# Kernel tuning notes

Hardware: AMD Instinct MI355X
Metric: run time of the kernel (lower is better)

Reference implementation:

```python
import jax, jax.numpy as jnp
import numpy as np

N, E, G, T = 4096, 16384, 128, 100
DIMS = [(5, 64), (64, 128), (128, 256)]
EPS = 1e-5


def setup_inputs() -> dict:
    key = jax.random.key(0)
    ks = iter(jax.random.split(key, 64))
    d = {}
    d["x"] = jax.random.normal(next(ks), (N, 5), jnp.float32)
    d["edge_index"] = jax.random.randint(next(ks), (2, E), 0, N, jnp.int64)
    d["edge_attr"] = jax.random.uniform(next(ks), (E, 3), jnp.float32)
    d["batch_seg"] = jnp.sort(jax.random.randint(next(ks), (N,), 0, G, jnp.int64))
    for l, (cin, cout) in enumerate(DIMS, start=1):
        d[f"l{l}_W1"] = jax.random.normal(next(ks), (3, 32), jnp.float32) * 0.3
        d[f"l{l}_b1"] = jnp.zeros((32,), jnp.float32)
        d[f"l{l}_W2"] = jax.random.normal(next(ks), (32, cin * cout), jnp.float32) * 0.05
        d[f"l{l}_b2"] = jnp.zeros((cin * cout,), jnp.float32)
        d[f"l{l}_root"] = jax.random.normal(next(ks), (cin, cout), jnp.float32) * 0.1
        d[f"l{l}_bias"] = jnp.zeros((cout,), jnp.float32)
        d[f"bn{l}_g"] = jnp.ones((cout,), jnp.float32)
        d[f"bn{l}_b"] = jnp.zeros((cout,), jnp.float32)
        d[f"bn{l}_m"] = jax.random.normal(next(ks), (cout,), jnp.float32) * 0.01
        d[f"bn{l}_v"] = jax.random.uniform(next(ks), (cout,), jnp.float32, 0.5, 1.5)
    d["mlp_W"] = jax.random.normal(next(ks), (256, T), jnp.float32) * 0.06
    d["mlp_b"] = jnp.zeros((T,), jnp.float32)
    return d


def _nnconv(h, src, dst, edge_attr, W1, b1, W2, b2, root, bias, cin, cout):
    # edge MLP -> per-edge weight matrix [E, cin, cout]
    ew = (jax.nn.relu(edge_attr @ W1 + b1) @ W2 + b2).reshape(-1, cin, cout)
    msg = jnp.einsum('ei,eio->eo', h[src], ew)  # gather + per-edge matmul
    ssum = jax.ops.segment_sum(msg, dst, num_segments=N)
    cnt = jax.ops.segment_sum(jnp.ones((msg.shape[0],), msg.dtype), dst, num_segments=N)
    agg = ssum / jnp.maximum(cnt, 1.0)[:, None]  # scatter-mean
    return h @ root + agg + bias


def _bn(h, g, b, m, v):
    return g * (h - m) * jax.lax.rsqrt(v + EPS) + b


def reference(x, edge_index, edge_attr, batch_seg,
              l1_W1, l1_b1, l1_W2, l1_b2, l1_root, l1_bias, bn1_g, bn1_b, bn1_m, bn1_v,
              l2_W1, l2_b1, l2_W2, l2_b2, l2_root, l2_bias, bn2_g, bn2_b, bn2_m, bn2_v,
              l3_W1, l3_b1, l3_W2, l3_b2, l3_root, l3_bias, bn3_g, bn3_b, bn3_m, bn3_v,
              mlp_W, mlp_b):
    src, dst = edge_index[0], edge_index[1]
    h = _nnconv(x, src, dst, edge_attr, l1_W1, l1_b1, l1_W2, l1_b2, l1_root, l1_bias, 5, 64)
    h = jax.nn.relu(_bn(h, bn1_g, bn1_b, bn1_m, bn1_v))
    h = _nnconv(h, src, dst, edge_attr, l2_W1, l2_b1, l2_W2, l2_b2, l2_root, l2_bias, 64, 128)
    h = jax.nn.relu(_bn(h, bn2_g, bn2_b, bn2_m, bn2_v))
    h = _nnconv(h, src, dst, edge_attr, l3_W1, l3_b1, l3_W2, l3_b2, l3_root, l3_bias, 128, 256)
    h = jax.nn.relu(_bn(h, bn3_g, bn3_b, bn3_m, bn3_v))
    # global mean pool over graphs
    psum = jax.ops.segment_sum(h, batch_seg, num_segments=G)
    pcnt = jax.ops.segment_sum(jnp.ones((N,), h.dtype), batch_seg, num_segments=G)
    pooled = psum / jnp.maximum(pcnt, 1.0)[:, None]
    out = pooled @ mlp_W + mlp_b
    return jnp.where(out > 0, out, 0.1 * out)  # LeakyReLU(0.1)
```

## Files before the change

kernel.cpp:

```cpp
#include <hip/hip_runtime.h>
#include <cstdint>
#include <cstddef>

#define BN_EPS 1e-5f

typedef short bf16x8 __attribute__((ext_vector_type(8)));
typedef float f32x4  __attribute__((ext_vector_type(4)));
typedef unsigned short u16x8 __attribute__((ext_vector_type(8)));

__device__ __forceinline__ uint16_t f2bf_rte(float f) {
  uint32_t u = __float_as_uint(f);
  uint32_t r = u + 0x7fffu + ((u >> 16) & 1u);
  return (uint16_t)(r >> 16);
}
__device__ __forceinline__ float bf2f(uint16_t h) {
  return __uint_as_float(((uint32_t)h) << 16);
}
__device__ __forceinline__ void split_bf(float v, uint16_t& hi, uint16_t& lo) {
  hi = f2bf_rte(v);
  lo = f2bf_rte(v - bf2f(hi));
}

__global__ void zero_i32_k(int* p, int n) {
  int i = blockIdx.x * blockDim.x + threadIdx.x;
  if (i < n) p[i] = 0;
}

__global__ void hist_k(const int* __restrict__ dst, int* __restrict__ cnt, int E) {
  int e = blockIdx.x * blockDim.x + threadIdx.x;
  if (e < E) atomicAdd(&cnt[dst[e]], 1);
}

__global__ __launch_bounds__(1024) void scan_k(const int* __restrict__ cnt,
                                               int* __restrict__ offsets,
                                               int* __restrict__ cursor,
                                               int N, int total) {
  __shared__ int part[1024];
  int t = threadIdx.x;
  int a0 = cnt[4*t+0], a1 = cnt[4*t+1], a2 = cnt[4*t+2], a3 = cnt[4*t+3];
  part[t] = a0 + a1 + a2 + a3;
  __syncthreads();
  for (int off = 1; off < 1024; off <<= 1) {
    int v = (t >= off) ? part[t - off] : 0;
    __syncthreads();
    part[t] += v;
    __syncthreads();
  }
  int excl = (t == 0) ? 0 : part[t-1];
  int o0 = excl, o1 = o0 + a0, o2 = o1 + a1, o3 = o2 + a2;
  offsets[4*t+0] = o0; offsets[4*t+1] = o1; offsets[4*t+2] = o2; offsets[4*t+3] = o3;
  cursor [4*t+0] = o0; cursor [4*t+1] = o1; cursor [4*t+2] = o2; cursor [4*t+3] = o3;
  if (t == 0) offsets[N] = total;
}

__global__ void scatter_k(const int* __restrict__ dst, int* __restrict__ cursor,
                          int* __restrict__ csr, int E) {
  int e = blockIdx.x * blockDim.x + threadIdx.x;
  if (e < E) {
    int d = dst[e];
    int pos = atomicAdd(&cursor[d], 1);
    csr[pos] = e;
  }
}

__global__ void build_W2pT_k(const float* __restrict__ W2, const float* __restrict__ b2,
                             const float* __restrict__ root,
                             uint16_t* __restrict__ Bhi, uint16_t* __restrict__ Blo,
                             int cin, int cout, int Kpad) {
  int idx = blockIdx.x * blockDim.x + threadIdx.x;
  int total = cout * Kpad;
  if (idx >= total) return;
  int o  = idx / Kpad;
  int ki = idx - o * Kpad;
  float v = 0.f;
  if (ki < 34 * cin) {
    int k = ki / cin;
    int i = ki - k * cin;
    if (k < 32)       v = W2[(size_t)k * cin * cout + (size_t)i * cout + o];
    else if (k == 32) v = b2[(size_t)i * cout + o];
    else              v = root[(size_t)i * cout + o];
  }
  uint16_t hi, lo;
  split_bf(v, hi, lo);
  Bhi[idx] = hi;
  Blo[idx] = lo;
}

template<int CIN>
__global__ __launch_bounds__(256) void build_S_vec_k(const float* __restrict__ h,
                                                     const float* __restrict__ ea,
                                                     const float* __restrict__ W1,
                                                     const float* __restrict__ b1,
                                                     const int* __restrict__ src,
                                                     const int* __restrict__ csr,
                                                     const int* __restrict__ offsets,
                                                     uint16_t* __restrict__ Shi,
                                                     uint16_t* __restrict__ Slo,
                                                     int Kpad) {
  constexpr int CH = 8;
  constexpr int K1 = 33 * CIN;
  constexpr int NCH = K1 / 8;
  constexpr int NP = (NCH + 255) / 256;
  __shared__ float hs[CH][CIN];
  __shared__ float zs[CH][33];
  __shared__ int   es[CH];
  const int n = blockIdx.x;
  const int tid = threadIdx.x;
  const int base = offsets[n];
  const int deg  = offsets[n+1] - base;
  const float scale = 1.f / fmaxf((float)deg, 1.f);
  float acc[NP][8];
#pragma unroll
  for (int p = 0; p < NP; p++)
#pragma unroll
    for (int j = 0; j < 8; j++) acc[p][j] = 0.f;

  for (int c0 = 0; c0 < deg; c0 += CH) {
    const int cc = min(CH, deg - c0);
    if (tid < cc) es[tid] = csr[base + c0 + tid];
    __syncthreads();
    for (int idx = tid; idx < cc * CIN; idx += 256) {
      int slot = idx / CIN, i = idx - slot * CIN;
      hs[slot][i] = h[(size_t)src[es[slot]] * CIN + i];
    }
    for (int idx = tid; idx < cc * 33; idx += 256) {
      int slot = idx / 33, k = idx - slot * 33;
      float v;
      if (k == 32) v = 1.f;
      else {
        int e = es[slot];
        v = fmaxf(ea[e*3+0] * W1[k] + ea[e*3+1] * W1[32 + k] + ea[e*3+2] * W1[64 + k] + b1[k], 0.f);
      }
      zs[slot][k] = v;
    }
    __syncthreads();
#pragma unroll
    for (int p = 0; p < NP; p++) {
      int ch = p * 256 + tid;
      if (ch < NCH) {
        int ki0 = ch * 8;
        int k  = ki0 / CIN;
        int i0 = ki0 & (CIN - 1);
        for (int c = 0; c < cc; c++) {
          float zv = zs[c][k];
          float4 h0 = *(const float4*)&hs[c][i0];
          float4 h1 = *(const float4*)&hs[c][i0 + 4];
          acc[p][0] += zv * h0.x; acc[p][1] += zv * h0.y;
          acc[p][2] += zv * h0.z; acc[p][3] += zv * h0.w;
          acc[p][4] += zv * h1.x; acc[p][5] += zv * h1.y;
          acc[p][6] += zv * h1.z; acc[p][7] += zv * h1.w;
        }
      }
    }
    __syncthreads();
  }
  const size_t rowb = (size_t)n * Kpad;
#pragma unroll
  for (int p = 0; p < NP; p++) {
    int ch = p * 256 + tid;
    if (ch < NCH) {
      u16x8 hv, lv;
#pragma unroll
      for (int j = 0; j < 8; j++) {
        uint16_t hi, lo;
        split_bf(acc[p][j] * scale, hi, lo);
        hv[j] = hi; lv[j] = lo;
      }
      *(u16x8*)(Shi + rowb + ch * 8) = hv;
      *(u16x8*)(Slo + rowb + ch * 8) = lv;
    }
  }
  for (int c = tid; c < CIN / 8; c += 256) {
    int i0 = c * 8;
    float4 a = *(const float4*)&h[(size_t)n * CIN + i0];
    float4 b = *(const float4*)&h[(size_t)n * CIN + i0 + 4];
    float vals[8] = {a.x, a.y, a.z, a.w, b.x, b.y, b.z, b.w};
    u16x8 hv, lv;
#pragma unroll
    for (int j = 0; j < 8; j++) {
      uint16_t hi, lo;
      split_bf(vals[j], hi, lo);
      hv[j] = hi; lv[j] = lo;
    }
    *(u16x8*)(Shi + rowb + K1 + i0) = hv;
    *(u16x8*)(Slo + rowb + K1 + i0) = lv;
  }
  for (int ki = 34 * CIN + tid; ki < Kpad; ki += 256) {
    Shi[rowb + ki] = 0;
    Slo[rowb + ki] = 0;
  }
}

__global__ __launch_bounds__(256) void build_S5_k(const float* __restrict__ h,
                                                  const float* __restrict__ ea,
                                                  const float* __restrict__ W1,
                                                  const float* __restrict__ b1,
                                                  const int* __restrict__ src,
                                                  const int* __restrict__ csr,
                                                  const int* __restrict__ offsets,
                                                  uint16_t* __restrict__ Shi,
                                                  uint16_t* __restrict__ Slo,
                                                  int Kpad) {
  constexpr int CIN = 5, CH = 8;
  constexpr int K1 = 33 * CIN;
  constexpr int KT = 34 * CIN;
  __shared__ float hs[CH][CIN];
  __shared__ float zs[CH][33];
  __shared__ int   es[CH];
  const int n = blockIdx.x;
  const int tid = threadIdx.x;
  const int base = offsets[n];
  const int deg  = offsets[n+1] - base;
  const float scale = 1.f / fmaxf((float)deg, 1.f);
  float acc = 0.f;

  for (int c0 = 0; c0 < deg; c0 += CH) {
    const int cc = min(CH, deg - c0);
    if (tid < cc) es[tid] = csr[base + c0 + tid];
    __syncthreads();
    for (int idx = tid; idx < cc * CIN; idx += 256) {
      int slot = idx / CIN, i = idx - slot * CIN;
      hs[slot][i] = h[(size_t)src[es[slot]] * CIN + i];
    }
    for (int idx = tid; idx < cc * 33; idx += 256) {
      int slot = idx / 33, k = idx - slot * 33;
      float v;
      if (k == 32) v = 1.f;
      else {
        int e = es[slot];
        v = fmaxf(ea[e*3+0] * W1[k] + ea[e*3+1] * W1[32 + k] + ea[e*3+2] * W1[64 + k] + b1[k], 0.f);
      }
      zs[slot][k] = v;
    }
    __syncthreads();
    if (tid < K1) {
      int k = tid / CIN, i = tid - (tid / CIN) * CIN;
      float a = acc;
      for (int c = 0; c < cc; c++) a += zs[c][k] * hs[c][i];
      acc = a;
    }
    __syncthreads();
  }
  const size_t rowb = (size_t)n * Kpad;
  if (tid < K1) {
    uint16_t hi, lo;
    split_bf(acc * scale, hi, lo);
    Shi[rowb + tid] = hi;
    Slo[rowb + tid] = lo;
  }
  if (tid < CIN) {
    uint16_t hi, lo;
    split_bf(h[(size_t)n * CIN + tid], hi, lo);
    Shi[rowb + K1 + tid] = hi;
    Slo[rowb + K1 + tid] = lo;
  }
  for (int ki = KT + tid; ki < Kpad; ki += 256) {
    Shi[rowb + ki] = 0;
    Slo[rowb + ki] = 0;
  }
}

__global__ __launch_bounds__(256, 4) void mfma_gemm_sk_k(const uint16_t* __restrict__ Ahi,
                                                         const uint16_t* __restrict__ Alo,
                                                         const uint16_t* __restrict__ Bhi,
                                                         const uint16_t* __restrict__ Blo,
                                                         float* __restrict__ Cpart,
                                                         int Kpad, int Ncol, int M,
                                                         int itersPerSplit) {
  __shared__ uint16_t As[2][64][72];
  __shared__ uint16_t Bs[2][64][72];
  const int m0 = blockIdx.x * 64, n0 = blockIdx.y * 64;
  const int kbeg = blockIdx.z * itersPerSplit * 64;
  const int kend = min(Kpad, kbeg + itersPerSplit * 64);
  const int tid  = threadIdx.x;
  const int lane = tid & 63;
  const int wave = tid >> 6;
  const int wm = wave & 1, wn = wave >> 1;
  const int q  = lane >> 4;
  const int mr = lane & 15;

  f32x4 acc[2][2];
#pragma unroll
  for (int a = 0; a < 2; a++)
#pragma unroll
    for (int b = 0; b < 2; b++) acc[a][b] = (f32x4)0.f;

  for (int k0 = kbeg; k0 < kend; k0 += 64) {
#pragma unroll
    for (int rep = 0; rep < 2; rep++) {
      int chunk = rep * 256 + tid;
      int r = chunk >> 3, c = chunk & 7;
      size_t ga = (size_t)(m0 + r) * Kpad + k0 + c * 8;
      size_t gb = (size_t)(n0 + r) * Kpad + k0 + c * 8;
      *(uint4*)&As[0][r][c * 8] = *(const uint4*)(Ahi + ga);
      *(uint4*)&As[1][r][c * 8] = *(const uint4*)(Alo + ga);
      *(uint4*)&Bs[0][r][c * 8] = *(const uint4*)(Bhi + gb);
      *(uint4*)&Bs[1][r][c * 8] = *(const uint4*)(Blo + gb);
    }
    __syncthreads();
#pragma unroll
    for (int ks = 0; ks < 2; ks++) {
      const int kb = ks * 32 + q * 8;
      bf16x8 ah[2], al[2], bh[2], bl[2];
#pragma unroll
      for (int f = 0; f < 2; f++) {
        ah[f] = *(const bf16x8*)&As[0][wm * 32 + f * 16 + mr][kb];
        al[f] = *(const bf16x8*)&As[1][wm * 32 + f * 16 + mr][kb];
        bh[f] = *(const bf16x8*)&Bs[0][wn * 32 + f * 16 + mr][kb];
        bl[f] = *(const bf16x8*)&Bs[1][wn * 32 + f * 16 + mr][kb];
      }
#pragma unroll
      for (int fm = 0; fm < 2; fm++)
#pragma unroll
        for (int fn = 0; fn < 2; fn++) {
          acc[fm][fn] = __builtin_amdgcn_mfma_f32_16x16x32_bf16(ah[fm], bh[fn], acc[fm][fn], 0, 0, 0);
          acc[fm][fn] = __builtin_amdgcn_mfma_f32_16x16x32_bf16(ah[fm], bl[fn], acc[fm][fn], 0, 0, 0);
          acc[fm][fn] = __builtin_amdgcn_mfma_f32_16x16x32_bf16(al[fm], bh[fn], acc[fm][fn], 0, 0, 0);
        }
    }
    __syncthreads();
  }

  float* Cz = Cpart + (size_t)blockIdx.z * M * Ncol;
#pragma unroll
  for (int fm = 0; fm < 2; fm++) {
#pragma unroll
    for (int reg = 0; reg < 4; reg++) {
      int row = m0 + wm * 32 + fm * 16 + q * 4 + reg;
#pragma unroll
      for (int fn = 0; fn < 2; fn++) {
        int col = n0 + wn * 32 + fn * 16 + mr;
        Cz[(size_t)row * Ncol + col] = acc[fm][fn][reg];
      }
    }
  }
}

__global__ void epilogue_k(const float* __restrict__ Cpart, int SK, size_t plane4,
                           int Ncol,
                           const float* __restrict__ bias, const float* __restrict__ bg,
                           const float* __restrict__ bb, const float* __restrict__ bnm,
                           const float* __restrict__ bnv,
                           float* __restrict__ C, int total4) {
  int i = blockIdx.x * blockDim.x + threadIdx.x;
  if (i >= total4) return;
  float4 v = {0.f, 0.f, 0.f, 0.f};
  for (int z = 0; z < SK; z++) {
    float4 p = *((const float4*)Cpart + (size_t)z * plane4 + i);
    v.x += p.x; v.y += p.y; v.z += p.z; v.w += p.w;
  }
  int col0 = (i * 4) % Ncol;
  float o[4] = {v.x, v.y, v.z, v.w};
#pragma unroll
  for (int j = 0; j < 4; j++) {
    int c = col0 + j;
    float s = bg[c] * rsqrtf(bnv[c] + BN_EPS);
    float val = (o[j] + bias[c] - bnm[c]) * s + bb[c];
    o[j] = fmaxf(val, 0.f);
  }
  float4 r = {o[0], o[1], o[2], o[3]};
  *((float4*)C + i) = r;
}

__global__ __launch_bounds__(256) void pool_final_k(const float* __restrict__ h,
                                                    const int* __restrict__ seg,
                                                    const float* __restrict__ W,
                                                    const float* __restrict__ b,
                                                    float* __restrict__ out,
                                                    int N, int T) {
  __shared__ float pooled[256];
  const int g = blockIdx.x, tid = threadIdx.x;
  int lo = 0, hi = N;
  while (lo < hi) { int mid = (lo + hi) >> 1; if (seg[mid] < g) lo = mid + 1; else hi = mid; }
  int lo2 = lo, hi2 = N;
  while (lo2 < hi2) { int mid = (lo2 + hi2) >> 1; if (seg[mid] < g + 1) lo2 = mid + 1; else hi2 = mid; }
  const int cnt = lo2 - lo;
  const float inv = 1.f / fmaxf((float)cnt, 1.f);
  float s = 0.f;
  for (int n = lo; n < lo2; n++) s += h[(size_t)n * 256 + tid];
  pooled[tid] = s * inv;
  __syncthreads();
  if (tid < T) {
    float acc = b[tid];
    for (int o = 0; o < 256; o++) acc += pooled[o] * W[(size_t)o * T + tid];
    out[(size_t)g * T + tid] = (acc > 0.f) ? acc : 0.1f * acc;
  }
}

extern "C" void kernel_launch(void* const* d_in, const int* in_sizes, int n_in,
                              void* d_out, int out_size, void* d_ws, size_t ws_size,
                              hipStream_t stream) {
  const float* x   = (const float*)d_in[0];
  const int*   ei  = (const int*)d_in[1];
  const float* ea  = (const float*)d_in[2];
  const int*   seg = (const int*)d_in[3];

  const int N = in_sizes[0] / 5;
  const int E = in_sizes[2] / 3;
  const int T = in_sizes[35];
  const int G = out_size / T;
  const int* src = ei;
  const int* dst = ei + E;

  const float *W1[3], *b1[3], *W2[3], *b2[3], *root[3], *bias[3];
  const float *bng[3], *bnb[3], *bnm[3], *bnv[3];
  for (int l = 0; l < 3; l++) {
    int base = 4 + l * 10;
    W1[l]   = (const float*)d_in[base + 0];
    b1[l]   = (const float*)d_in[base + 1];
    W2[l]   = (const float*)d_in[base + 2];
    b2[l]   = (const float*)d_in[base + 3];
    root[l] = (const float*)d_in[base + 4];
    bias[l] = (const float*)d_in[base + 5];
    bng[l]  = (const float*)d_in[base + 6];
    bnb[l]  = (const float*)d_in[base + 7];
    bnm[l]  = (const float*)d_in[base + 8];
    bnv[l]  = (const float*)d_in[base + 9];
  }
  const float* mlpW = (const float*)d_in[34];
  const float* mlpb = (const float*)d_in[35];

  char* p = (char*)d_ws;
  auto carve = [&](size_t bytes) -> char* {
    char* r = p;
    p += (bytes + 255) & ~(size_t)255;
    return r;
  };
  const int KPADMAX = 4352;
  const int SKMAX = 8;
  int*      cnt     = (int*)carve((size_t)N * 4);
  int*      offsets = (int*)carve((size_t)(N + 1) * 4);
  int*      cursor  = (int*)carve((size_t)N * 4);
  int*      csr     = (int*)carve((size_t)E * 4);
  uint16_t* Whi     = (uint16_t*)carve((size_t)256 * KPADMAX * 2);
  uint16_t* Wlo     = (uint16_t*)carve((size_t)256 * KPADMAX * 2);
  uint16_t* Shi     = (uint16_t*)carve((size_t)N * KPADMAX * 2);
  uint16_t* Slo     = (uint16_t*)carve((size_t)N * KPADMAX * 2);
  float*    Cpart   = (float*)carve((size_t)SKMAX * N * 256 * 4 / 2);
  float*    hA      = (float*)carve((size_t)N * 256 * 4);
  float*    hB      = (float*)carve((size_t)N * 128 * 4);

  zero_i32_k<<<(N + 255) / 256, 256, 0, stream>>>(cnt, N);
  hist_k<<<(E + 255) / 256, 256, 0, stream>>>(dst, cnt, E);
  scan_k<<<1, 1024, 0, stream>>>(cnt, offsets, cursor, N, E);
  scatter_k<<<(E + 255) / 256, 256, 0, stream>>>(dst, cursor, csr, E);

  const int cins[3]  = {5, 64, 128};
  const int couts[3] = {64, 128, 256};
  const int kpads[3] = {192, 2176, 4352};
  const int sks[3]   = {1, 8, 4};
  const float* hin = x;
  float* houts[3] = {hB, hB, hA};
  houts[0] = hA; houts[1] = hB; houts[2] = hA;

  for (int l = 0; l < 3; l++) {
    int cin = cins[l], cout = couts[l], Kpad = kpads[l], SK = sks[l];
    int iters = Kpad / 64;
    int ips = (iters + SK - 1) / SK;
    build_W2pT_k<<<(cout * Kpad + 255) / 256, 256, 0, stream>>>(W2[l], b2[l], root[l],
                                                                Whi, Wlo, cin, cout, Kpad);
    if (cin == 5)
      build_S5_k<<<N, 256, 0, stream>>>(hin, ea, W1[l], b1[l], src, csr, offsets, Shi, Slo, Kpad);
    else if (cin == 64)
      build_S_vec_k<64><<<N, 256, 0, stream>>>(hin, ea, W1[l], b1[l], src, csr, offsets, Shi, Slo, Kpad);
    else
      build_S_vec_k<128><<<N, 256, 0, stream>>>(hin, ea, W1[l], b1[l], src, csr, offsets, Shi, Slo, Kpad);
    dim3 grid(N / 64, cout / 64, SK);
    mfma_gemm_sk_k<<<grid, 256, 0, stream>>>(Shi, Slo, Whi, Wlo, Cpart, Kpad, cout, N, ips);
    int total4 = N * cout / 4;
    epilogue_k<<<(total4 + 255) / 256, 256, 0, stream>>>(Cpart, SK, (size_t)N * cout / 4, cout,
                                                         bias[l], bng[l], bnb[l], bnm[l], bnv[l],
                                                         houts[l], total4);
    hin = houts[l];
  }

  pool_final_k<<<G, 256, 0, stream>>>(hA, seg, mlpW, mlpb, (float*)d_out, N, T);
}
```

Baseline: 285.8 us.

## Rewrite split-K MFMA GEMM with larger tiles, direct-to-LDS loads and double buffering

Replaces the 64x64 split-K bf16x3 GEMM with a templated 128xBN tile kernel. It stages A and B through global_load_lds into XOR-swizzled, double-buffered shared memory, so the next K-step's loads overlap the current MFMAs and each iteration needs one barrier instead of two. Split-K ranges are now divided evenly, and layer 1 uses split 3 so a smaller grid still fills the GPU. Larger tiles raise data reuse per load but increase register and LDS use, which lowers occupancy. The swizzle and the LDS-load addressing must match exactly for the results to be correct.

```diff
diff --git a/kernel.cpp b/kernel.cpp
--- a/kernel.cpp
+++ b/kernel.cpp
@@ -19,6 +19,12 @@
 __device__ __forceinline__ void split_bf(float v, uint16_t& hi, uint16_t& lo) {
   hi = f2bf_rte(v);
   lo = f2bf_rte(v - bf2f(hi));
+}
+
+__device__ __forceinline__ void glds16(const uint16_t* g, uint16_t* l) {
+  __builtin_amdgcn_global_load_lds(
+      (const __attribute__((address_space(1))) uint32_t*)(const void*)g,
+      (__attribute__((address_space(3))) uint32_t*)(void*)l, 16, 0, 0);
 }
 
 __global__ void zero_i32_k(int* p, int n) {
@@ -260,18 +266,33 @@
   }
 }
 
-__global__ __launch_bounds__(256, 4) void mfma_gemm_sk_k(const uint16_t* __restrict__ Ahi,
-                                                         const uint16_t* __restrict__ Alo,
-                                                         const uint16_t* __restrict__ Bhi,
-                                                         const uint16_t* __restrict__ Blo,
-                                                         float* __restrict__ Cpart,
-                                                         int Kpad, int Ncol, int M,
-                                                         int itersPerSplit) {
-  __shared__ uint16_t As[2][64][72];
-  __shared__ uint16_t Bs[2][64][72];
-  const int m0 = blockIdx.x * 64, n0 = blockIdx.y * 64;
-  const int kbeg = blockIdx.z * itersPerSplit * 64;
-  const int kend = min(Kpad, kbeg + itersPerSplit * 64);
+template<int BN>
+__global__ __launch_bounds__(256) void mfma_gemm2_k(const uint16_t* __restrict__ Ahi,
+                                                    const uint16_t* __restrict__ Alo,
+                                                    const uint16_t* __restrict__ Bhi,
+                                                    const uint16_t* __restrict__ Blo,
+                                                    float* __restrict__ Cpart,
+                                                    int Kpad, int Ncol, int M,
+                                                    int totalIters) {
+  constexpr int BM = 128;
+  constexpr int FN = BN / 32;
+  constexpr int NCA = BM / 32;
+  constexpr int NCB = BN / 32;
+  constexpr int OAH = 0;
+  constexpr int OAL = BM * 64;
+  constexpr int OBH = 2 * BM * 64;
+  constexpr int OBL = 2 * BM * 64 + BN * 64;
+  constexpr int BUFSZ = (2 * BM + 2 * BN) * 64;
+  __shared__ uint16_t smem[2 * BUFSZ] __attribute__((aligned(16)));
+
+  const int m0 = blockIdx.x * BM;
+  const int n0 = blockIdx.y * BN;
+  const int SK = gridDim.z;
+  const int z  = blockIdx.z;
+  const int itBeg = (int)((long long)totalIters * z / SK);
+  const int itEnd = (int)((long long)totalIters * (z + 1) / SK);
+  const int nsteps = itEnd - itBeg;
+
   const int tid  = threadIdx.x;
   const int lane = tid & 63;
   const int wave = tid >> 6;
@@ -279,61 +300,82 @@
   const int q  = lane >> 4;
   const int mr = lane & 15;
 
-  f32x4 acc[2][2];
-#pragma unroll
-  for (int a = 0; a < 2; a++)
-#pragma unroll
-    for (int b = 0; b < 2; b++) acc[a][b] = (f32x4)0.f;
-
-  for (int k0 = kbeg; k0 < kend; k0 += 64) {
-#pragma unroll
-    for (int rep = 0; rep < 2; rep++) {
-      int chunk = rep * 256 + tid;
-      int r = chunk >> 3, c = chunk & 7;
-      size_t ga = (size_t)(m0 + r) * Kpad + k0 + c * 8;
-      size_t gb = (size_t)(n0 + r) * Kpad + k0 + c * 8;
-      *(uint4*)&As[0][r][c * 8] = *(const uint4*)(Ahi + ga);
-      *(uint4*)&As[1][r][c * 8] = *(const uint4*)(Alo + ga);
-      *(uint4*)&Bs[0][r][c * 8] = *(const uint4*)(Bhi + gb);
-      *(uint4*)&Bs[1][r][c * 8] = *(const uint4*)(Blo + gb);
-    }
-    __syncthreads();
+  const int srow = tid >> 3;
+  const int swz  = ((tid & 7) ^ (srow & 7)) << 3;
+  size_t aoff[NCA], boff[NCB];
+#pragma unroll
+  for (int c = 0; c < NCA; c++)
+    aoff[c] = (size_t)(m0 + c * 32 + srow) * Kpad + swz + (size_t)itBeg * 64;
+#pragma unroll
+  for (int c = 0; c < NCB; c++)
+    boff[c] = (size_t)(n0 + c * 32 + srow) * Kpad + swz + (size_t)itBeg * 64;
+  const int wlds = wave << 9;
+
+  f32x4 acc[4][FN];
+#pragma unroll
+  for (int a = 0; a < 4; a++)
+#pragma unroll
+    for (int b = 0; b < FN; b++) acc[a][b] = (f32x4)0.f;
+
+  auto stage = [&](int buf, int t) {
+    uint16_t* base = smem + buf * BUFSZ;
+    const size_t ka = (size_t)t * 64;
+#pragma unroll
+    for (int c = 0; c < NCA; c++) {
+      glds16(Ahi + aoff[c] + ka, base + OAH + c * 2048 + wlds);
+      glds16(Alo + aoff[c] + ka, base + OAL + c * 2048 + wlds);
+    }
+#pragma unroll
+    for (int c = 0; c < NCB; c++) {
+      glds16(Bhi + boff[c] + ka, base + OBH + c * 2048 + wlds);
+      glds16(Blo + boff[c] + ka, base + OBL + c * 2048 + wlds);
+    }
+  };
+
+  if (nsteps > 0) stage(0, 0);
+  for (int t = 0; t < nsteps; t++) {
+    __syncthreads();
+    if (t + 1 < nsteps) stage((t & 1) ^ 1, t + 1);
+    const uint16_t* B_ = smem + (t & 1) * BUFSZ;
 #pragma unroll
     for (int ks = 0; ks < 2; ks++) {
-      const int kb = ks * 32 + q * 8;
-      bf16x8 ah[2], al[2], bh[2], bl[2];
-#pragma unroll
-      for (int f = 0; f < 2; f++) {
-        ah[f] = *(const bf16x8*)&As[0][wm * 32 + f * 16 + mr][kb];
-        al[f] = *(const bf16x8*)&As[1][wm * 32 + f * 16 + mr][kb];
-        bh[f] = *(const bf16x8*)&Bs[0][wn * 32 + f * 16 + mr][kb];
-        bl[f] = *(const bf16x8*)&Bs[1][wn * 32 + f * 16 + mr][kb];
-      }
-#pragma unroll
-      for (int fm = 0; fm < 2; fm++)
-#pragma unroll
-        for (int fn = 0; fn < 2; fn++) {
+      const int e0 = (ks * 32 + q * 8) ^ ((mr & 7) << 3);
+      bf16x8 ah[4], al[4], bh[FN], bl[FN];
+#pragma unroll
+      for (int f = 0; f < 4; f++) {
+        const int row = wm * 64 + f * 16 + mr;
+        ah[f] = *(const bf16x8*)&B_[OAH + row * 64 + e0];
+        al[f] = *(const bf16x8*)&B_[OAL + row * 64 + e0];
+      }
+#pragma unroll
+      for (int f = 0; f < FN; f++) {
+        const int row = wn * (BN / 2) + f * 16 + mr;
+        bh[f] = *(const bf16x8*)&B_[OBH + row * 64 + e0];
+        bl[f] = *(const bf16x8*)&B_[OBL + row * 64 + e0];
+      }
+#pragma unroll
+      for (int fm = 0; fm < 4; fm++)
+#pragma unroll
+        for (int fn = 0; fn < FN; fn++) {
           acc[fm][fn] = __builtin_amdgcn_mfma_f32_16x16x32_bf16(ah[fm], bh[fn], acc[fm][fn], 0, 0, 0);
           acc[fm][fn] = __builtin_amdgcn_mfma_f32_16x16x32_bf16(ah[fm], bl[fn], acc[fm][fn], 0, 0, 0);
           acc[fm][fn] = __builtin_amdgcn_mfma_f32_16x16x32_bf16(al[fm], bh[fn], acc[fm][fn], 0, 0, 0);
         }
     }
-    __syncthreads();
-  }
-
-  float* Cz = Cpart + (size_t)blockIdx.z * M * Ncol;
-#pragma unroll
-  for (int fm = 0; fm < 2; fm++) {
+  }
+
+  float* Cz = Cpart + (size_t)z * M * Ncol;
+#pragma unroll
+  for (int fm = 0; fm < 4; fm++)
 #pragma unroll
     for (int reg = 0; reg < 4; reg++) {
-      int row = m0 + wm * 32 + fm * 16 + q * 4 + reg;
-#pragma unroll
-      for (int fn = 0; fn < 2; fn++) {
-        int col = n0 + wn * 32 + fn * 16 + mr;
+      const int row = m0 + wm * 64 + fm * 16 + q * 4 + reg;
+#pragma unroll
+      for (int fn = 0; fn < FN; fn++) {
+        const int col = n0 + wn * (BN / 2) + fn * 16 + mr;
         Cz[(size_t)row * Ncol + col] = acc[fm][fn][reg];
       }
     }
-  }
 }
 
 __global__ void epilogue_k(const float* __restrict__ Cpart, int SK, size_t plane4,
@@ -448,15 +490,14 @@
   const int cins[3]  = {5, 64, 128};
   const int couts[3] = {64, 128, 256};
   const int kpads[3] = {192, 2176, 4352};
-  const int sks[3]   = {1, 8, 4};
+  const int sks[3]   = {3, 8, 4};
+
   const float* hin = x;
-  float* houts[3] = {hB, hB, hA};
-  houts[0] = hA; houts[1] = hB; houts[2] = hA;
+  float* houts[3] = {hA, hB, hA};
 
   for (int l = 0; l < 3; l++) {
     int cin = cins[l], cout = couts[l], Kpad = kpads[l], SK = sks[l];
     int iters = Kpad / 64;
-    int ips = (iters + SK - 1) / SK;
     build_W2pT_k<<<(cout * Kpad + 255) / 256, 256, 0, stream>>>(W2[l], b2[l], root[l],
                                                                 Whi, Wlo, cin, cout, Kpad);
     if (cin == 5)
@@ -465,8 +506,17 @@
       build_S_vec_k<64><<<N, 256, 0, stream>>>(hin, ea, W1[l], b1[l], src, csr, offsets, Shi, Slo, Kpad);
     else
       build_S_vec_k<128><<<N, 256, 0, stream>>>(hin, ea, W1[l], b1[l], src, csr, offsets, Shi, Slo, Kpad);
-    dim3 grid(N / 64, cout / 64, SK);
-    mfma_gemm_sk_k<<<grid, 256, 0, stream>>>(Shi, Slo, Whi, Wlo, Cpart, Kpad, cout, N, ips);
+
+    if (cout >= 128) {
+      dim3 grid(N / 128, cout / 128, SK);
+      mfma_gemm2_k<128><<<grid, 256, 0, stream>>>(Shi, Slo, Whi, Wlo, Cpart,
+                                                  Kpad, cout, N, iters);
+    } else {
+      dim3 grid(N / 128, 1, SK);
+      mfma_gemm2_k<64><<<grid, 256, 0, stream>>>(Shi, Slo, Whi, Wlo, Cpart,
+                                                 Kpad, cout, N, iters);
+    }
+
     int total4 = N * cout / 4;
     epilogue_k<<<(total4 + 255) / 256, 256, 0, stream>>>(Cpart, SK, (size_t)N * cout / 4, cout,
                                                          bias[l], bng[l], bnb[l], bnm[l], bnv[l],
```

Result: faster. 279.8 us (-2.1%).
